# Performance work log

Measured on AMD Instinct MI355X. Metric: run time of the kernel, lower is better.

## Reference

```python
import jax, jax.numpy as jnp
import numpy as np

N = 100000   # nodes
E = 1000000  # edges
D = 64       # in_features
D_OUT = 64   # out_features


def setup_inputs() -> dict:
    key = jax.random.key(0)
    k1, k2, k3, k4, k5, k6 = jax.random.split(key, 6)
    h = jax.random.normal(k1, (N, D), dtype=jnp.float32)          # current node features ndata['h']
    i = jax.random.normal(k2, (N, D), dtype=jnp.float32)          # initial features ndata['i']
    edge_src = jax.random.randint(k3, (E,), 0, N, dtype=jnp.int32)
    edge_dst = jax.random.randint(k4, (E,), 0, N, dtype=jnp.int32)
    edge_w = jax.random.uniform(k5, (E,), dtype=jnp.float32)      # scalar edge weight edata['x']
    stdv = 1.0 / np.sqrt(D_OUT)
    weight = jax.random.uniform(k6, (2 * D, D_OUT), dtype=jnp.float32,
                                minval=-stdv, maxval=stdv)        # variant=True -> in = 2*D
    return {
        "h": h, "i": i, "weight": weight, "edge_w": edge_w,
        "lamda": jnp.float32(0.5), "alpha": jnp.float32(0.1),
        "edge_src": edge_src, "edge_dst": edge_dst, "layer_idx": 4,
    }


def reference(h, i, weight, edge_w, lamda, alpha, edge_src, edge_dst, layer_idx):
    # theta = min(1, log(lamda/layer_idx + 1))
    theta = jnp.minimum(jnp.float32(1.0), jnp.log(lamda / layer_idx + 1.0))
    # update_all(u_mul_e('h','x','m'), sum('m','h')): edge-weighted gather-scatter SpMM
    m = h[edge_src] * edge_w[:, None]                 # [E, D]
    h_agg = jax.ops.segment_sum(m, edge_dst, num_segments=h.shape[0])  # [N, D]
    # variant=True branch
    support = jnp.concatenate([h_agg, i], axis=1)     # [N, 2D]
    r = (1.0 - alpha) * h_agg + alpha * i             # [N, D]
    out = theta * (support @ weight) + (1.0 - theta) * r
    # residual=True
    out = out + i
    return out
```

## Files before the change

### kernel.cpp

```cpp
#include <hip/hip_runtime.h>
#include <math.h>


#define DFEAT 64
#define BINSZ 128
#define NBINS 1024
#define CAP   2048
#define CHUNK 4096
#define TPB   512
#define ASTR  72

typedef unsigned long long u64;
typedef __attribute__((ext_vector_type(8))) short bf16x8;
typedef __attribute__((ext_vector_type(4))) float f32x4;

__device__ inline unsigned short to_bf16(float f) {
    unsigned u = __float_as_uint(f);
    u += 0x7FFF + ((u >> 16) & 1);
    return (unsigned short)(u >> 16);
}
__device__ inline float bf_up(unsigned short s) {
    return __uint_as_float(((unsigned)s) << 16);
}

__global__ __launch_bounds__(512) void bin_fill_kernel(
    const float* __restrict__ h, const float* __restrict__ weight,
    const int* __restrict__ e_src, const int* __restrict__ e_dst,
    const float* __restrict__ e_w, int* __restrict__ gcur,
    u64* __restrict__ bucket, ushort* __restrict__ h16,
    ushort* __restrict__ w16, int E, int total4) {
    __shared__ u64 staging[CHUNK];
    __shared__ unsigned short binOf[CHUNK];
    __shared__ int hist[NBINS], offs[NBINS], gbase[NBINS], cur[NBINS];
    __shared__ int part[TPB];

    int tid = threadIdx.x;
    int gid = blockIdx.x * TPB + tid;
    int nthreads = gridDim.x * TPB;

    for (int i = gid; i < total4; i += nthreads) {
        float4 v = ((const float4*)h)[i];
        ushort4 o;
        o.x = to_bf16(v.x); o.y = to_bf16(v.y);
        o.z = to_bf16(v.z); o.w = to_bf16(v.w);
        ((ushort4*)h16)[i] = o;
    }
    if (gid < 8192) {
        int j = gid & 7, l = (gid >> 3) & 63, cs = gid >> 9;
        int c = cs >> 2, s = cs & 3, q = l >> 4, m = l & 15;
        w16[gid] = to_bf16(weight[(s * 32 + q * 8 + j) * DFEAT + c * 16 + m]);
    }

    int e0 = blockIdx.x * CHUNK;
    int cc = min(CHUNK, E - e0);

    hist[tid] = 0; hist[tid + 512] = 0;
    __syncthreads();

    int d[8], s[8];
    float w[8];
#pragma unroll
    for (int j = 0; j < 8; ++j) {
        int e = e0 + j * TPB + tid;
        if (e < E) { d[j] = e_dst[e]; s[j] = e_src[e]; w[j] = e_w[e]; }
        else d[j] = -1;
    }
#pragma unroll
    for (int j = 0; j < 8; ++j)
        if (d[j] >= 0) atomicAdd(&hist[d[j] >> 7], 1);
    __syncthreads();

    int a = hist[2 * tid], b = hist[2 * tid + 1];
    part[tid] = a + b;
    __syncthreads();
    for (int ofs = 1; ofs < TPB; ofs <<= 1) {
        int t = (tid >= ofs) ? part[tid - ofs] : 0;
        __syncthreads();
        part[tid] += t;
        __syncthreads();
    }
    int excl = part[tid] - (a + b);
    offs[2 * tid] = excl;         cur[2 * tid] = excl;
    offs[2 * tid + 1] = excl + a; cur[2 * tid + 1] = excl + a;
    __syncthreads();

#pragma unroll
    for (int j = 0; j < 8; ++j) {
        if (d[j] >= 0) {
            int bb = d[j] >> 7;
            int p = atomicAdd(&cur[bb], 1);
            unsigned lo = (unsigned)s[j] | ((unsigned)(d[j] & 127) << 24);
            staging[p] = ((u64)(unsigned)__float_as_int(w[j]) << 32) | lo;
            binOf[p] = (unsigned short)bb;
        }
    }
    __syncthreads();

    for (int t = tid; t < NBINS; t += TPB) {
        int c = hist[t];
        gbase[t] = (c > 0) ? atomicAdd(&gcur[t], c) : 0;
    }
    __syncthreads();

#pragma unroll
    for (int j = 0; j < 8; ++j) {
        int p = j * TPB + tid;
        if (p < cc) {
            int bb = binOf[p];
            bucket[(size_t)bb * CAP + gbase[bb] + (p - offs[bb])] = staging[p];
        }
    }
}

__global__ __launch_bounds__(512) void spmm_kernel(
    const ushort* __restrict__ h16, const u64* __restrict__ bucket,
    const int* __restrict__ gcur, const ushort* __restrict__ w16,
    const float* __restrict__ ifeat,
    const float* __restrict__ lamda_p, const float* __restrict__ alpha_p,
    const int* __restrict__ layer_p,
    float* __restrict__ out, int N) {
    __shared__ u64 sorted[CAP];
    __shared__ __align__(16) ushort agg16[BINSZ * ASTR];
    __shared__ int hist[BINSZ], start[BINSZ], cur[BINSZ], part[BINSZ];

    int tid = threadIdx.x;
    int bin = blockIdx.x;
    int base = bin << 7;
    int cnt = gcur[bin];
    const u64* bk = bucket + (size_t)bin * CAP;

    if (tid < BINSZ) hist[tid] = 0;
    __syncthreads();

    for (int p = tid; p < cnt; p += TPB)
        atomicAdd(&hist[(((unsigned)bk[p]) >> 24) & 127], 1);
    __syncthreads();

    int v = 0;
    if (tid < BINSZ) { v = hist[tid]; part[tid] = v; }
    __syncthreads();
    for (int ofs = 1; ofs < BINSZ; ofs <<= 1) {
        int t = (tid < BINSZ && tid >= ofs) ? part[tid - ofs] : 0;
        __syncthreads();
        if (tid < BINSZ) part[tid] += t;
        __syncthreads();
    }
    if (tid < BINSZ) { start[tid] = part[tid] - v; cur[tid] = part[tid] - v; }
    __syncthreads();

    for (int p = tid; p < cnt; p += TPB) {
        u64 e = bk[p];
        int pos = atomicAdd(&cur[(((unsigned)e) >> 24) & 127], 1);
        sorted[pos] = e;
    }
    __syncthreads();

    int lane = tid & 63, wv = tid >> 6;
    int g = lane >> 4, m = lane & 15;
    int nn = min(BINSZ, N - base);

    for (int k = 0; k < 16; ++k) {
        int nl = wv * 16 + k;
        if (nl >= nn) break;
        int d = hist[nl];
        int b0 = start[nl];
        float a0 = 0.f, a1 = 0.f, a2 = 0.f, a3 = 0.f;
        for (int t0 = 0; t0 < d; t0 += 16) {
#pragma unroll
            for (int s = 0; s < 4; ++s) {
                int idx = t0 + s * 4 + g;
                u64 e = sorted[b0 + min(idx, d - 1)];
                float wt = (idx < d) ? __int_as_float((int)(e >> 32)) : 0.f;
                int src = ((unsigned)e) & 0xFFFFFF;
                ushort4 hv = *(const ushort4*)(h16 + (size_t)src * DFEAT + m * 4);
                a0 += wt * bf_up(hv.x);
                a1 += wt * bf_up(hv.y);
                a2 += wt * bf_up(hv.z);
                a3 += wt * bf_up(hv.w);
            }
        }
        a0 += __shfl_xor(a0, 16); a1 += __shfl_xor(a1, 16);
        a2 += __shfl_xor(a2, 16); a3 += __shfl_xor(a3, 16);
        a0 += __shfl_xor(a0, 32); a1 += __shfl_xor(a1, 32);
        a2 += __shfl_xor(a2, 32); a3 += __shfl_xor(a3, 32);
        if (g == 0) {
            ushort4 o;
            o.x = to_bf16(a0); o.y = to_bf16(a1);
            o.z = to_bf16(a2); o.w = to_bf16(a3);
            *(ushort4*)(agg16 + nl * ASTR + m * 4) = o;
        }
    }

    float alf = alpha_p[0];
    float theta = fminf(1.0f, logf(lamda_p[0] / (float)layer_p[0] + 1.0f));
    int q = lane >> 4;

    bf16x8 faA[2], faI[2];
#pragma unroll
    for (int s = 0; s < 2; ++s)
        faA[s] = *(const bf16x8*)(agg16 + (wv * 16 + m) * ASTR + s * 32 + q * 8);
    {
        const float* ip = ifeat + (size_t)min(base + wv * 16 + m, N - 1) * DFEAT;
#pragma unroll
        for (int s = 0; s < 2; ++s) {
            float4 v0 = *(const float4*)(ip + s * 32 + q * 8);
            float4 v1 = *(const float4*)(ip + s * 32 + q * 8 + 4);
            bf16x8 t;
            t[0] = (short)to_bf16(v0.x); t[1] = (short)to_bf16(v0.y);
            t[2] = (short)to_bf16(v0.z); t[3] = (short)to_bf16(v0.w);
            t[4] = (short)to_bf16(v1.x); t[5] = (short)to_bf16(v1.y);
            t[6] = (short)to_bf16(v1.z); t[7] = (short)to_bf16(v1.w);
            faI[s] = t;
        }
    }

    f32x4 acc[4] = {{0.f, 0.f, 0.f, 0.f}, {0.f, 0.f, 0.f, 0.f},
                    {0.f, 0.f, 0.f, 0.f}, {0.f, 0.f, 0.f, 0.f}};
#pragma unroll
    for (int c = 0; c < 4; ++c) {
#pragma unroll
        for (int s = 0; s < 2; ++s) {
            bf16x8 bA = *(const bf16x8*)(w16 + ((c * 4 + s) * 64 + lane) * 8);
            acc[c] = __builtin_amdgcn_mfma_f32_16x16x32_bf16(faA[s], bA, acc[c], 0, 0, 0);
            bf16x8 bI = *(const bf16x8*)(w16 + ((c * 4 + s + 2) * 64 + lane) * 8);
            acc[c] = __builtin_amdgcn_mfma_f32_16x16x32_bf16(faI[s], bI, acc[c], 0, 0, 0);
        }
    }

#pragma unroll
    for (int c = 0; c < 4; ++c) {
        int col = c * 16 + m;
#pragma unroll
        for (int r = 0; r < 4; ++r) {
            int rowL = wv * 16 + q * 4 + r;
            int row = base + rowL;
            if (row < N) {
                float av = bf_up(agg16[rowL * ASTR + col]);
                float iv = ifeat[(size_t)row * DFEAT + col];
                out[(size_t)row * DFEAT + col] =
                    theta * acc[c][r] +
                    (1.f - theta) * ((1.f - alf) * av + alf * iv) + iv;
            }
        }
    }
}

extern "C" void kernel_launch(void* const* d_in, const int* in_sizes, int n_in,
                              void* d_out, int out_size, void* d_ws, size_t ws_size,
                              hipStream_t stream) {
    const float* h       = (const float*)d_in[0];
    const float* ifeat   = (const float*)d_in[1];
    const float* weight  = (const float*)d_in[2];
    const float* edge_w  = (const float*)d_in[3];
    const float* lamda_p = (const float*)d_in[4];
    const float* alpha_p = (const float*)d_in[5];
    const int*   e_src   = (const int*)d_in[6];
    const int*   e_dst   = (const int*)d_in[7];
    const int*   layer_p = (const int*)d_in[8];
    float* out = (float*)d_out;

    int N = in_sizes[0] / DFEAT;
    int E = in_sizes[3];
    int nbins = (N + BINSZ - 1) >> 7;

    int* gcur = (int*)d_ws;
    u64* bucket = (u64*)((char*)d_ws + 4096);
    ushort* h16 = (ushort*)((char*)bucket + (size_t)NBINS * CAP * sizeof(u64));
    ushort* w16 = h16 + (size_t)N * DFEAT;

    hipMemsetAsync(gcur, 0, NBINS * sizeof(int), stream);

    int total4 = N * DFEAT / 4;
    bin_fill_kernel<<<(E + CHUNK - 1) / CHUNK, TPB, 0, stream>>>(
        h, weight, e_src, e_dst, edge_w, gcur, bucket, h16, w16, E, total4);

    spmm_kernel<<<nbins, TPB, 0, stream>>>(
        h16, bucket, gcur, w16, ifeat, lamda_p, alpha_p, layer_p, out, N);
}
```

Before: 163.0 us.

## Switch to fp16 packed accumulation, split bins into half-blocks, separate conversion kernel

Replaces the bf16 storage and fp32 scalar accumulation with fp16 storage and packed half2 FMA accumulation, and uses the f16 MFMA. The spmm grid is doubled: each block handles 64 destination nodes of a 128-node bin, filtering the bucket twice and using a wave-shuffle scan instead of an LDS scan. The h/weight conversion is moved out of bin_fill into its own kernel. These changes aim for more parallelism and cheaper inner-loop arithmetic. The cost is fp16 accumulation precision and overflow risk, redundant bucket reads, and an extra launch.

```diff
diff --git a/kernel.cpp b/kernel.cpp
--- a/kernel.cpp
+++ b/kernel.cpp
@@ -1,4 +1,5 @@
 #include <hip/hip_runtime.h>
+#include <hip/hip_fp16.h>
 #include <math.h>
 
 
@@ -6,51 +7,54 @@
 #define BINSZ 128
 #define NBINS 1024
 #define CAP   2048
+#define SUBSZ 64
+#define SCAP  1024
 #define CHUNK 4096
 #define TPB   512
+
 #define ASTR  72
 
 typedef unsigned long long u64;
-typedef __attribute__((ext_vector_type(8))) short bf16x8;
+typedef __attribute__((ext_vector_type(8))) _Float16 f16x8;
 typedef __attribute__((ext_vector_type(4))) float f32x4;
 
-__device__ inline unsigned short to_bf16(float f) {
-    unsigned u = __float_as_uint(f);
-    u += 0x7FFF + ((u >> 16) & 1);
-    return (unsigned short)(u >> 16);
-}
-__device__ inline float bf_up(unsigned short s) {
-    return __uint_as_float(((unsigned)s) << 16);
+__device__ inline unsigned h2u(__half2 h) {
+    union { __half2 h; unsigned u; } c; c.h = h; return c.u;
+}
+__device__ inline __half2 u2h(unsigned u) {
+    union { unsigned u; __half2 h; } c; c.u = u; return c.h;
+}
+
+__global__ __launch_bounds__(256) void convert_kernel(
+    const float* __restrict__ h, const float* __restrict__ weight,
+    ushort* __restrict__ h16, ushort* __restrict__ w16, int total4) {
+    int gid = blockIdx.x * 256 + threadIdx.x;
+    int nth = gridDim.x * 256;
+    for (int i = gid; i < total4; i += nth) {
+        float4 v = ((const float4*)h)[i];
+        uint2 o;
+        o.x = h2u(__floats2half2_rn(v.x, v.y));
+        o.y = h2u(__floats2half2_rn(v.z, v.w));
+        ((uint2*)h16)[i] = o;
+    }
+    if (gid < 8192) {
+        int j = gid & 7, l = (gid >> 3) & 63, cs = gid >> 9;
+        int c = cs >> 2, s = cs & 3, q = l >> 4, m = l & 15;
+        w16[gid] = __half_as_ushort(
+            __float2half_rn(weight[(s * 32 + q * 8 + j) * DFEAT + c * 16 + m]));
+    }
 }
 
 __global__ __launch_bounds__(512) void bin_fill_kernel(
-    const float* __restrict__ h, const float* __restrict__ weight,
     const int* __restrict__ e_src, const int* __restrict__ e_dst,
     const float* __restrict__ e_w, int* __restrict__ gcur,
-    u64* __restrict__ bucket, ushort* __restrict__ h16,
-    ushort* __restrict__ w16, int E, int total4) {
+    u64* __restrict__ bucket, int E) {
     __shared__ u64 staging[CHUNK];
     __shared__ unsigned short binOf[CHUNK];
     __shared__ int hist[NBINS], offs[NBINS], gbase[NBINS], cur[NBINS];
     __shared__ int part[TPB];
 
     int tid = threadIdx.x;
-    int gid = blockIdx.x * TPB + tid;
-    int nthreads = gridDim.x * TPB;
-
-    for (int i = gid; i < total4; i += nthreads) {
-        float4 v = ((const float4*)h)[i];
-        ushort4 o;
-        o.x = to_bf16(v.x); o.y = to_bf16(v.y);
-        o.z = to_bf16(v.z); o.w = to_bf16(v.w);
-        ((ushort4*)h16)[i] = o;
-    }
-    if (gid < 8192) {
-        int j = gid & 7, l = (gid >> 3) & 63, cs = gid >> 9;
-        int c = cs >> 2, s = cs & 3, q = l >> 4, m = l & 15;
-        w16[gid] = to_bf16(weight[(s * 32 + q * 8 + j) * DFEAT + c * 16 + m]);
-    }
-
     int e0 = blockIdx.x * CHUNK;
     int cc = min(CHUNK, E - e0);
 
@@ -119,126 +123,135 @@
     const float* __restrict__ lamda_p, const float* __restrict__ alpha_p,
     const int* __restrict__ layer_p,
     float* __restrict__ out, int N) {
-    __shared__ u64 sorted[CAP];
-    __shared__ __align__(16) ushort agg16[BINSZ * ASTR];
-    __shared__ int hist[BINSZ], start[BINSZ], cur[BINSZ], part[BINSZ];
+    __shared__ u64 sorted[SCAP];
+    __shared__ __align__(16) ushort agg16[SUBSZ * ASTR];
+    __shared__ int hist[SUBSZ], start[SUBSZ], cur[SUBSZ];
 
     int tid = threadIdx.x;
-    int bin = blockIdx.x;
-    int base = bin << 7;
+    int bin = blockIdx.x >> 1;
+    int half = blockIdx.x & 1;
+    int lo = half << 6;
+    int base = (bin << 7) + lo;
     int cnt = gcur[bin];
     const u64* bk = bucket + (size_t)bin * CAP;
 
-    if (tid < BINSZ) hist[tid] = 0;
-    __syncthreads();
-
-    for (int p = tid; p < cnt; p += TPB)
-        atomicAdd(&hist[(((unsigned)bk[p]) >> 24) & 127], 1);
-    __syncthreads();
-
-    int v = 0;
-    if (tid < BINSZ) { v = hist[tid]; part[tid] = v; }
-    __syncthreads();
-    for (int ofs = 1; ofs < BINSZ; ofs <<= 1) {
-        int t = (tid < BINSZ && tid >= ofs) ? part[tid - ofs] : 0;
-        __syncthreads();
-        if (tid < BINSZ) part[tid] += t;
-        __syncthreads();
-    }
-    if (tid < BINSZ) { start[tid] = part[tid] - v; cur[tid] = part[tid] - v; }
+    if (tid < SUBSZ) hist[tid] = 0;
+    __syncthreads();
+
+    for (int p = tid; p < cnt; p += TPB) {
+        int dl = (int)((((unsigned)bk[p]) >> 24) & 127);
+        if ((dl & 64) == lo) atomicAdd(&hist[dl & 63], 1);
+    }
+    __syncthreads();
+
+    if (tid < 64) {
+        int v = hist[tid];
+        int s = v;
+#pragma unroll
+        for (int ofs = 1; ofs < 64; ofs <<= 1) {
+            int t = __shfl_up(s, ofs);
+            if (tid >= ofs) s += t;
+        }
+        start[tid] = s - v;
+        cur[tid] = s - v;
+    }
     __syncthreads();
 
     for (int p = tid; p < cnt; p += TPB) {
         u64 e = bk[p];
-        int pos = atomicAdd(&cur[(((unsigned)e) >> 24) & 127], 1);
-        sorted[pos] = e;
+        int dl = (int)((((unsigned)e) >> 24) & 127);
+        if ((dl & 64) == lo) {
+            int pos = atomicAdd(&cur[dl & 63], 1);
+            sorted[pos] = e;
+        }
     }
     __syncthreads();
 
     int lane = tid & 63, wv = tid >> 6;
     int g = lane >> 4, m = lane & 15;
-    int nn = min(BINSZ, N - base);
-
-    for (int k = 0; k < 16; ++k) {
-        int nl = wv * 16 + k;
+    int nn = min(SUBSZ, N - base);
+
+    for (int k = 0; k < 8; ++k) {
+        int nl = (wv << 3) + k;
         if (nl >= nn) break;
         int d = hist[nl];
         int b0 = start[nl];
-        float a0 = 0.f, a1 = 0.f, a2 = 0.f, a3 = 0.f;
+        __half2 a01 = u2h(0u), a23 = u2h(0u);
         for (int t0 = 0; t0 < d; t0 += 16) {
 #pragma unroll
             for (int s = 0; s < 4; ++s) {
-                int idx = t0 + s * 4 + g;
+                int idx = t0 + (s << 2) + g;
                 u64 e = sorted[b0 + min(idx, d - 1)];
-                float wt = (idx < d) ? __int_as_float((int)(e >> 32)) : 0.f;
-                int src = ((unsigned)e) & 0xFFFFFF;
-                ushort4 hv = *(const ushort4*)(h16 + (size_t)src * DFEAT + m * 4);
-                a0 += wt * bf_up(hv.x);
-                a1 += wt * bf_up(hv.y);
-                a2 += wt * bf_up(hv.z);
-                a3 += wt * bf_up(hv.w);
+                float wf = (idx < d) ? __int_as_float((int)(e >> 32)) : 0.f;
+                __half2 w2 = __float2half2_rn(wf);
+                unsigned src = ((unsigned)e) & 0xFFFFFFu;
+                uint2 hv = *(const uint2*)(h16 + ((size_t)src << 6) + (m << 2));
+                a01 = __hfma2(w2, u2h(hv.x), a01);
+                a23 = __hfma2(w2, u2h(hv.y), a23);
             }
         }
-        a0 += __shfl_xor(a0, 16); a1 += __shfl_xor(a1, 16);
-        a2 += __shfl_xor(a2, 16); a3 += __shfl_xor(a3, 16);
-        a0 += __shfl_xor(a0, 32); a1 += __shfl_xor(a1, 32);
-        a2 += __shfl_xor(a2, 32); a3 += __shfl_xor(a3, 32);
+        a01 = __hadd2(a01, u2h((unsigned)__shfl_xor((int)h2u(a01), 16)));
+        a23 = __hadd2(a23, u2h((unsigned)__shfl_xor((int)h2u(a23), 16)));
+        a01 = __hadd2(a01, u2h((unsigned)__shfl_xor((int)h2u(a01), 32)));
+        a23 = __hadd2(a23, u2h((unsigned)__shfl_xor((int)h2u(a23), 32)));
         if (g == 0) {
-            ushort4 o;
-            o.x = to_bf16(a0); o.y = to_bf16(a1);
-            o.z = to_bf16(a2); o.w = to_bf16(a3);
-            *(ushort4*)(agg16 + nl * ASTR + m * 4) = o;
-        }
-    }
+            uint2 o; o.x = h2u(a01); o.y = h2u(a23);
+            *(uint2*)(agg16 + nl * ASTR + (m << 2)) = o;
+        }
+    }
+    __syncthreads();
 
     float alf = alpha_p[0];
     float theta = fminf(1.0f, logf(lamda_p[0] / (float)layer_p[0] + 1.0f));
-    int q = lane >> 4;
-
-    bf16x8 faA[2], faI[2];
+    int q = g;
+    int t = wv >> 1, ch = wv & 1;
+
+    f16x8 faA[2], faI[2];
 #pragma unroll
     for (int s = 0; s < 2; ++s)
-        faA[s] = *(const bf16x8*)(agg16 + (wv * 16 + m) * ASTR + s * 32 + q * 8);
+        faA[s] = *(const f16x8*)(agg16 + (t * 16 + m) * ASTR + s * 32 + q * 8);
     {
-        const float* ip = ifeat + (size_t)min(base + wv * 16 + m, N - 1) * DFEAT;
+        const float* ip = ifeat + (size_t)min(base + t * 16 + m, N - 1) * DFEAT;
 #pragma unroll
         for (int s = 0; s < 2; ++s) {
             float4 v0 = *(const float4*)(ip + s * 32 + q * 8);
             float4 v1 = *(const float4*)(ip + s * 32 + q * 8 + 4);
-            bf16x8 t;
-            t[0] = (short)to_bf16(v0.x); t[1] = (short)to_bf16(v0.y);
-            t[2] = (short)to_bf16(v0.z); t[3] = (short)to_bf16(v0.w);
-            t[4] = (short)to_bf16(v1.x); t[5] = (short)to_bf16(v1.y);
-            t[6] = (short)to_bf16(v1.z); t[7] = (short)to_bf16(v1.w);
-            faI[s] = t;
-        }
-    }
-
-    f32x4 acc[4] = {{0.f, 0.f, 0.f, 0.f}, {0.f, 0.f, 0.f, 0.f},
-                    {0.f, 0.f, 0.f, 0.f}, {0.f, 0.f, 0.f, 0.f}};
-#pragma unroll
-    for (int c = 0; c < 4; ++c) {
+            f16x8 tt;
+            tt[0] = (_Float16)v0.x; tt[1] = (_Float16)v0.y;
+            tt[2] = (_Float16)v0.z; tt[3] = (_Float16)v0.w;
+            tt[4] = (_Float16)v1.x; tt[5] = (_Float16)v1.y;
+            tt[6] = (_Float16)v1.z; tt[7] = (_Float16)v1.w;
+            faI[s] = tt;
+        }
+    }
+
+    f32x4 acc[2] = {{0.f, 0.f, 0.f, 0.f}, {0.f, 0.f, 0.f, 0.f}};
+#pragma unroll
+    for (int ci = 0; ci < 2; ++ci) {
+        int c = ch * 2 + ci;
 #pragma unroll
         for (int s = 0; s < 2; ++s) {
-            bf16x8 bA = *(const bf16x8*)(w16 + ((c * 4 + s) * 64 + lane) * 8);
-            acc[c] = __builtin_amdgcn_mfma_f32_16x16x32_bf16(faA[s], bA, acc[c], 0, 0, 0);
-            bf16x8 bI = *(const bf16x8*)(w16 + ((c * 4 + s + 2) * 64 + lane) * 8);
-            acc[c] = __builtin_amdgcn_mfma_f32_16x16x32_bf16(faI[s], bI, acc[c], 0, 0, 0);
-        }
-    }
-
-#pragma unroll
-    for (int c = 0; c < 4; ++c) {
+            f16x8 bA = *(const f16x8*)(w16 + ((c * 4 + s) * 64 + lane) * 8);
+            acc[ci] = __builtin_amdgcn_mfma_f32_16x16x32_f16(faA[s], bA, acc[ci], 0, 0, 0);
+            f16x8 bI = *(const f16x8*)(w16 + ((c * 4 + s + 2) * 64 + lane) * 8);
+            acc[ci] = __builtin_amdgcn_mfma_f32_16x16x32_f16(faI[s], bI, acc[ci], 0, 0, 0);
+        }
+    }
+
+#pragma unroll
+    for (int ci = 0; ci < 2; ++ci) {
+        int c = ch * 2 + ci;
         int col = c * 16 + m;
 #pragma unroll
         for (int r = 0; r < 4; ++r) {
-            int rowL = wv * 16 + q * 4 + r;
+            int rowL = t * 16 + q * 4 + r;
             int row = base + rowL;
             if (row < N) {
-                float av = bf_up(agg16[rowL * ASTR + col]);
+                float av = __half2float(
+                    *(const __half*)(agg16 + rowL * ASTR + col));
                 float iv = ifeat[(size_t)row * DFEAT + col];
                 out[(size_t)row * DFEAT + col] =
-                    theta * acc[c][r] +
+                    theta * acc[ci][r] +
                     (1.f - theta) * ((1.f - alf) * av + alf * iv) + iv;
             }
         }
@@ -271,9 +284,11 @@
     hipMemsetAsync(gcur, 0, NBINS * sizeof(int), stream);
 
     int total4 = N * DFEAT / 4;
+    convert_kernel<<<2048, 256, 0, stream>>>(h, weight, h16, w16, total4);
+
     bin_fill_kernel<<<(E + CHUNK - 1) / CHUNK, TPB, 0, stream>>>(
-        h, weight, e_src, e_dst, edge_w, gcur, bucket, h16, w16, E, total4);
-
-    spmm_kernel<<<nbins, TPB, 0, stream>>>(
+        e_src, e_dst, edge_w, gcur, bucket, E);
+
+    spmm_kernel<<<nbins * 2, TPB, 0, stream>>>(
         h16, bucket, gcur, w16, ifeat, lamda_p, alpha_p, layer_p, out, N);
 }
```

Result: faster. 157.6 us (-3.3%).
